# Kernel tuning notes

Hardware: AMD Instinct MI355X
Metric: run time of the kernel (lower is better)

Reference implementation:

```python
import jax, jax.numpy as jnp
import numpy as np

B, N, H = 32, 512, 256


def setup_inputs() -> dict:
    key = jax.random.key(0)
    ks = jax.random.split(key, 10)
    s = 1.0 / np.sqrt(H)
    return {
        "encoder_outputs": jax.random.normal(ks[0], (B, N, H), jnp.float32),
        "W_ih": jax.random.normal(ks[1], (4 * H, H), jnp.float32) * s,  # LSTMCell input weights (i,f,g,o)
        "W_hh": jax.random.normal(ks[2], (4 * H, H), jnp.float32) * s,
        "b_ih": jnp.zeros((4 * H,), jnp.float32),
        "b_hh": jnp.zeros((4 * H,), jnp.float32),
        "W_a": jax.random.normal(ks[3], (H, H), jnp.float32) * s,  # attn_W_a (no bias)
        "U_a": jax.random.normal(ks[4], (H, H), jnp.float32) * s,  # attn_U_a (no bias)
        "v_a": jax.random.normal(ks[5], (H,), jnp.float32) * s,    # attn_v (H -> 1, no bias)
        "start_token": jax.random.uniform(ks[6], (H,), jnp.float32, -0.1, 0.1),
        "end_token": jax.random.uniform(ks[7], (H,), jnp.float32, -0.1, 0.1),
    }


def lstm_cell(x, h, c, W_ih, b_ih, W_hh, b_hh):
    gates = x @ W_ih.T + b_ih + h @ W_hh.T + b_hh  # [B, 4H], torch gate order i,f,g,o
    i, f, g, o = jnp.split(gates, 4, axis=-1)
    c2 = jax.nn.sigmoid(f) * c + jax.nn.sigmoid(i) * jnp.tanh(g)
    h2 = jax.nn.sigmoid(o) * jnp.tanh(c2)
    return h2, c2


def reference(encoder_outputs, W_ih, W_hh, b_ih, b_hh, W_a, U_a, v_a, start_token, end_token):
    batch, n_nodes, hidden = encoder_outputs.shape
    T = n_nodes + 1  # inference path: max_decoding_steps = num_input_nodes + 1
    # extended encoder outputs = [enc, end_token]; precompute W_a projection once
    ext = jnp.concatenate(
        [encoder_outputs, jnp.broadcast_to(end_token, (batch, 1, hidden))], axis=1
    )  # [B, T, H]
    enc_proj = jnp.einsum("bnh,kh->bnk", ext, W_a)  # [B, T, H]
    bidx = jnp.arange(batch)

    dec_in0 = jnp.broadcast_to(start_token, (batch, hidden))
    hx0 = jnp.zeros((batch, hidden), encoder_outputs.dtype)
    cx0 = jnp.zeros_like(hx0)
    mask0 = jnp.zeros((batch, T), encoder_outputs.dtype)

    def step(carry, _):
        dec_in, hx, cx, mask = carry
        hx, cx = lstm_cell(dec_in, hx, cx, W_ih, b_ih, W_hh, b_hh)
        q = hx @ U_a.T  # [B, H]
        scores = jnp.tanh(enc_proj + q[:, None, :]) @ v_a  # [B, T]
        scores = jnp.where(mask == 1, -jnp.inf, scores)
        scores = scores - jnp.max(scores, axis=1, keepdims=True)
        log_probs = jax.nn.log_softmax(scores, axis=1)  # [B, T]
        next_idx = jnp.argmax(log_probs, axis=1)  # greedy (no teacher forcing)
        sel = next_idx < n_nodes  # end token (idx == n_nodes) never gets masked
        mask = mask.at[bidx, next_idx].max(sel.astype(mask.dtype))
        gathered = encoder_outputs[bidx, jnp.minimum(next_idx, n_nodes - 1)]  # [B, H]
        dec_in = jnp.where(sel[:, None], gathered, end_token)
        return (dec_in, hx, cx, mask), (log_probs, next_idx)

    _, (outputs, selected) = jax.lax.scan(step, (dec_in0, hx0, cx0, mask0), None, length=T)
    return jnp.swapaxes(outputs, 0, 1), jnp.swapaxes(selected, 0, 1)  # [B,T,T], [B,T]
```

## Files before the change

kernel.cpp:

```cpp
#include <hip/hip_runtime.h>
#include <math.h>


#define NEG_BIG  (-1.0e30f)
#define SENTINEL (-3.0e38f)
#define L2E 1.4426950408889634f
#define C2T 2.8853900817779268f
#define LN2 0.6931471805599453f

#define OFF_CW   ((size_t)0)
#define OFF_ENCP ((size_t)327680)
#define OFF_BSUM ((size_t)4530176)
#define OFF_XW   ((size_t)4531200)
#define WS_END   ((size_t)21373952)
#define NEED_XW_BYTES (WS_END * 4)
#define SEL_OFF  ((size_t)(32u * 513u * 513u))

__device__ __forceinline__ float frcp(float x)  { float r; asm("v_rcp_f32 %0, %1" : "=v"(r) : "v"(x)); return r; }
__device__ __forceinline__ float fexp2(float x) { float r; asm("v_exp_f32 %0, %1" : "=v"(r) : "v"(x)); return r; }
__device__ __forceinline__ float flog2(float x) { float r; asm("v_log_f32 %0, %1" : "=v"(r) : "v"(x)); return r; }
__device__ __forceinline__ float fsig(float x)  { return frcp(1.f + fexp2(-L2E * x)); }
__device__ __forceinline__ float ftanh2(float x){ return fmaf(-2.f, frcp(fexp2(C2T * x) + 1.f), 1.f); }

__device__ __forceinline__ void bar_lgkm() {
  asm volatile("s_waitcnt lgkmcnt(0)\n\ts_barrier" ::: "memory");
}
__device__ __forceinline__ void bar_full() {
  asm volatile("s_waitcnt vmcnt(0) lgkmcnt(0)\n\ts_barrier" ::: "memory");
}

extern "C" __global__ void __launch_bounds__(256)
pd_proj(const float* __restrict__ enc,  const float* __restrict__ Wih,
        const float* __restrict__ Whh,  const float* __restrict__ bih,
        const float* __restrict__ bhh,  const float* __restrict__ Wa,
        const float* __restrict__ Ua,   const float* __restrict__ stok,
        const float* __restrict__ etok, float* __restrict__ ws, int ntA)
{
  __shared__ __align__(16) float smem[4352];
  const int tid = threadIdx.x;
  int bb = blockIdx.x;

  if (bb < ntA + 1028) {
    const bool isA = bb < ntA;
    const int tile = isA ? bb : bb - ntA;
    const int nTN  = isA ? 16 : 4;
    const int mt = tile / nTN, nt = tile % nTN;
    const int m0 = mt * 64, c0 = nt * 64;
    const float* Bmat = isA ? Wih : Wa;

    const int m_l = tid >> 2, kq = tid & 3;
    const int mrow = m0 + m_l;
    const int bA = mrow / 514, nA = mrow - bA * 514;
    const float* arow = (nA < 512) ? (enc + ((size_t)bA * 512 + nA) * 256)
                                   : (nA == 512 ? etok : stok);
    const float* brow = Bmat + (size_t)(c0 + m_l) * 256;
    float* As = smem; float* Bs = smem + 2176;
    const int ty = tid >> 4, tx = tid & 15;
    float acc[4][4] = {};

    for (int kc = 0; kc < 256; kc += 32) {
      __syncthreads();
      float4 a0 = ((const float4*)(arow + kc))[kq];
      float4 a1 = ((const float4*)(arow + kc))[kq + 4];
      float4 b0 = ((const float4*)(brow + kc))[kq];
      float4 b1 = ((const float4*)(brow + kc))[kq + 4];
      const int k0a = kq * 4;
      As[(k0a+0)*68 + m_l] = a0.x; As[(k0a+1)*68 + m_l] = a0.y;
      As[(k0a+2)*68 + m_l] = a0.z; As[(k0a+3)*68 + m_l] = a0.w;
      As[(16+k0a+0)*68 + m_l] = a1.x; As[(16+k0a+1)*68 + m_l] = a1.y;
      As[(16+k0a+2)*68 + m_l] = a1.z; As[(16+k0a+3)*68 + m_l] = a1.w;
      Bs[(k0a+0)*68 + m_l] = b0.x; Bs[(k0a+1)*68 + m_l] = b0.y;
      Bs[(k0a+2)*68 + m_l] = b0.z; Bs[(k0a+3)*68 + m_l] = b0.w;
      Bs[(16+k0a+0)*68 + m_l] = b1.x; Bs[(16+k0a+1)*68 + m_l] = b1.y;
      Bs[(16+k0a+2)*68 + m_l] = b1.z; Bs[(16+k0a+3)*68 + m_l] = b1.w;
      __syncthreads();
      #pragma unroll
      for (int k = 0; k < 32; ++k) {
        float4 a4 = *(const float4*)(As + k*68 + ty*4);
        float4 b4 = *(const float4*)(Bs + k*68 + tx*4);
        acc[0][0] = fmaf(a4.x, b4.x, acc[0][0]); acc[0][1] = fmaf(a4.x, b4.y, acc[0][1]);
        acc[0][2] = fmaf(a4.x, b4.z, acc[0][2]); acc[0][3] = fmaf(a4.x, b4.w, acc[0][3]);
        acc[1][0] = fmaf(a4.y, b4.x, acc[1][0]); acc[1][1] = fmaf(a4.y, b4.y, acc[1][1]);
        acc[1][2] = fmaf(a4.y, b4.z, acc[1][2]); acc[1][3] = fmaf(a4.y, b4.w, acc[1][3]);
        acc[2][0] = fmaf(a4.z, b4.x, acc[2][0]); acc[2][1] = fmaf(a4.z, b4.y, acc[2][1]);
        acc[2][2] = fmaf(a4.z, b4.z, acc[2][2]); acc[2][3] = fmaf(a4.z, b4.w, acc[2][3]);
        acc[3][0] = fmaf(a4.w, b4.x, acc[3][0]); acc[3][1] = fmaf(a4.w, b4.y, acc[3][1]);
        acc[3][2] = fmaf(a4.w, b4.z, acc[3][2]); acc[3][3] = fmaf(a4.w, b4.w, acc[3][3]);
      }
    }
    if (isA) {
      float b0 = bih[c0+tx*4+0] + bhh[c0+tx*4+0];
      float b1 = bih[c0+tx*4+1] + bhh[c0+tx*4+1];
      float b2 = bih[c0+tx*4+2] + bhh[c0+tx*4+2];
      float b3 = bih[c0+tx*4+3] + bhh[c0+tx*4+3];
      #pragma unroll
      for (int i = 0; i < 4; ++i) {
        int m = m0 + ty*4 + i; int bq = m / 514, n = m - bq * 514;
        float* d = ws + OFF_XW + ((size_t)bq*514 + n)*1024 + c0 + tx*4;
        d[0] = acc[i][0] + b0; d[1] = acc[i][1] + b1;
        d[2] = acc[i][2] + b2; d[3] = acc[i][3] + b3;
      }
    } else {
      #pragma unroll
      for (int i = 0; i < 4; ++i) {
        int m = m0 + ty*4 + i; int bq = m / 514, n = m - bq * 514;
        if (n < 513) {
          #pragma unroll
          for (int jj = 0; jj < 4; ++jj) {
            int j = c0 + tx*4 + jj;
            ws[OFF_ENCP + ((size_t)bq*256 + j)*513 + n] = fexp2(C2T * acc[i][jj]);
          }
        }
      }
    }
    return;
  }
  bb -= ntA + 1028;
  if (bb < 64) {
    const int kt = bb >> 4, rt = bb & 15;
    const int k0 = kt*64, r0 = rt*64;
    const int cl = tid & 63, rq = tid >> 6;
    for (int i = 0; i < 16; ++i) {
      int r = rq*16 + i;
      smem[r*65 + cl] = Whh[(size_t)(r0 + r)*256 + k0 + cl];
    }
    __syncthreads();
    for (int i = 0; i < 16; ++i) {
      int kk = k0 + rq*16 + i;
      ws[OFF_CW + (size_t)(kk >> 2)*5120 + (size_t)(r0 + cl)*4 + (kk & 3)]
          = smem[cl*65 + (rq*16 + i)];
    }
    return;
  }
  bb -= 64;
  if (bb < 16) {
    const int kt = bb >> 2, jt = bb & 3;
    const int k0 = kt*64, j0 = jt*64;
    const int cl = tid & 63, rq = tid >> 6;
    for (int i = 0; i < 16; ++i) {
      int j = rq*16 + i;
      smem[j*65 + cl] = Ua[(size_t)(j0 + j)*256 + k0 + cl];
    }
    __syncthreads();
    for (int i = 0; i < 16; ++i) {
      int kk = k0 + rq*16 + i;
      ws[OFF_CW + (size_t)(kk >> 2)*5120 + (size_t)(1024 + j0 + cl)*4 + (kk & 3)]
          = C2T * smem[cl*65 + (rq*16 + i)];
    }
    return;
  }
  for (int g = 0; g < 4; ++g)
    ws[OFF_BSUM + g*256 + tid] = bih[g*256 + tid] + bhh[g*256 + tid];
}

template<int USE_XW>
__global__ void __launch_bounds__(1024)
pd_decode(const float* __restrict__ enc, const float* __restrict__ Wih,
          const float* __restrict__ va,  const float* __restrict__ stok,
          const float* __restrict__ etok,
          float* __restrict__ out, float* __restrict__ ws)
{
  __shared__ __align__(16) float h_s[256];
  __shared__ __align__(16) float gpart[1024];
  __shared__ __align__(16) float qbuf[256];
  __shared__ __align__(16) float vbuf[256];
  __shared__ float maskb[513];
  __shared__ float spart[1040];
  __shared__ float redv[16];
  __shared__ int   redi[16];
  __shared__ int   sel_sh;
  __shared__ int   sel_flag;
  __shared__ int   cnt;

  const int tid  = threadIdx.x;
  const int b    = blockIdx.x;
  const int lane = tid & 63, w = tid >> 6;
  const float* cw = ws + OFF_CW;

  if (tid < 256) { h_s[tid] = 0.f; vbuf[tid] = va[tid]; }
  if (tid < 513) maskb[tid] = 0.f;
  gpart[tid] = 0.f;
  if (tid == 0) { sel_sh = 513; sel_flag = 0; cnt = 0; }
  float c_reg = 0.f;
  float bs0 = 0.f, bs1 = 0.f, bs2 = 0.f, bs3 = 0.f;
  if (!USE_XW && tid < 256) {
    bs0 = ws[OFF_BSUM + tid];       bs1 = ws[OFF_BSUM + 256 + tid];
    bs2 = ws[OFF_BSUM + 512 + tid]; bs3 = ws[OFF_BSUM + 768 + tid];
  }
  __syncthreads();

  const int nS = tid & 511, sS = tid >> 9;
  float sv = 0.f;
  #pragma unroll
  for (int j = 0; j < 32; ++j) {
    float4 v4 = *(const float4*)(vbuf + sS*128 + j*4);
    sv += v4.x + v4.y + v4.z + v4.w;
  }

  for (int t = 0; t < 513; ++t) {
    if (tid < 256) {
      int spins = 0;
      while (*(volatile int*)&sel_flag < t && ++spins < (1 << 22)) {}
      __threadfence_block();
      const int sel = *(volatile int*)&sel_sh;
      float xg0, xg1, xg2, xg3;
      if (USE_XW) {
        const float* xr = ws + OFF_XW + ((size_t)b*514 + sel)*1024 + tid;
        xg0 = xr[0]; xg1 = xr[256]; xg2 = xr[512]; xg3 = xr[768];
      } else {
        const float* xrow = (sel < 512) ? enc + ((size_t)b*512 + sel)*256
                                        : (sel == 512 ? etok : stok);
        const float4* x4 = (const float4*)xrow;
        xg0 = bs0; xg1 = bs1; xg2 = bs2; xg3 = bs3;
        #pragma unroll 2
        for (int k4 = 0; k4 < 64; ++k4) {
          float4 xv = x4[k4];
          float4 w0 = *(const float4*)(Wih + ((size_t)(tid      ))*256 + k4*4);
          float4 w1 = *(const float4*)(Wih + ((size_t)(256 + tid))*256 + k4*4);
          float4 w2 = *(const float4*)(Wih + ((size_t)(512 + tid))*256 + k4*4);
          float4 w3 = *(const float4*)(Wih + ((size_t)(768 + tid))*256 + k4*4);
          xg0 = fmaf(w0.x,xv.x,fmaf(w0.y,xv.y,fmaf(w0.z,xv.z,fmaf(w0.w,xv.w,xg0))));
          xg1 = fmaf(w1.x,xv.x,fmaf(w1.y,xv.y,fmaf(w1.z,xv.z,fmaf(w1.w,xv.w,xg1))));
          xg2 = fmaf(w2.x,xv.x,fmaf(w2.y,xv.y,fmaf(w2.z,xv.z,fmaf(w2.w,xv.w,xg2))));
          xg3 = fmaf(w3.x,xv.x,fmaf(w3.y,xv.y,fmaf(w3.z,xv.z,fmaf(w3.w,xv.w,xg3))));
        }
      }
      const float g0 = xg0 + gpart[tid];
      const float g1 = xg1 + gpart[256 + tid];
      const float g2 = xg2 + gpart[512 + tid];
      const float g3 = xg3 + gpart[768 + tid];
      const float cn = fsig(g1)*c_reg + fsig(g0)*ftanh2(g2);
      c_reg = cn;
      h_s[tid] = fsig(g3)*ftanh2(cn);
    }
    bar_lgkm();

    {
      float acc = 0.f;
      #pragma unroll 4
      for (int k4 = 0; k4 < 64; ++k4) {
        float4 h4 = *(const float4*)(h_s + k4*4);
        float4 wv = *(const float4*)(cw + (size_t)k4*5120 + (size_t)tid*4);
        acc = fmaf(wv.x,h4.x,fmaf(wv.y,h4.y,fmaf(wv.z,h4.z,fmaf(wv.w,h4.w,acc))));
      }
      gpart[tid] = acc;
      if (tid < 256) {
        float acc2 = 0.f;
        #pragma unroll 4
        for (int k4 = 0; k4 < 64; ++k4) {
          float4 h4 = *(const float4*)(h_s + k4*4);
          float4 wv = *(const float4*)(cw + (size_t)k4*5120 + (size_t)(1024 + tid)*4);
          acc2 = fmaf(wv.x,h4.x,fmaf(wv.y,h4.y,fmaf(wv.z,h4.z,fmaf(wv.w,h4.w,acc2))));
        }
        qbuf[tid] = fexp2(acc2);
      }
    }
    bar_lgkm();

    {
      const float* ET = ws + OFF_ENCP + ((size_t)b*256 + sS*128)*513 + nS;
      float sacc = 0.f;
      #pragma unroll 4
      for (int j4 = 0; j4 < 32; ++j4) {
        float4 F4 = *(const float4*)(qbuf + sS*128 + j4*4);
        float4 V4 = *(const float4*)(vbuf + sS*128 + j4*4);
        float e0 = ET[(size_t)(j4*4+0)*513];
        float e1 = ET[(size_t)(j4*4+1)*513];
        float e2 = ET[(size_t)(j4*4+2)*513];
        float e3 = ET[(size_t)(j4*4+3)*513];
        sacc = fmaf(V4.x, frcp(fmaf(e0, F4.x, 1.f)), sacc);
        sacc = fmaf(V4.y, frcp(fmaf(e1, F4.y, 1.f)), sacc);
        sacc = fmaf(V4.z, frcp(fmaf(e2, F4.z, 1.f)), sacc);
        sacc = fmaf(V4.w, frcp(fmaf(e3, F4.w, 1.f)), sacc);
      }
      spart[sS*520 + nS] = fmaf(-2.f, sacc, sv);
    }
    if (w == 0 || w == 8) {
      const int ss = w >> 3;
      const int j0 = ss*128 + lane*2;
      const float* er = ws + OFF_ENCP + ((size_t)b*256 + j0)*513 + 512;
      float a = vbuf[j0]   * frcp(fmaf(er[0],   qbuf[j0],   1.f))
              + vbuf[j0+1] * frcp(fmaf(er[513], qbuf[j0+1], 1.f));
      #pragma unroll
      for (int off = 1; off < 64; off <<= 1) a += __shfl_xor(a, off);
      if (lane == 0) spart[ss*520 + 512] = fmaf(-2.f, a, sv);
    }
    bar_lgkm();

    float val; int idx = tid;
    if (tid < 513) {
      float sc = spart[tid] + spart[520 + tid];
      if (maskb[tid] != 0.f) sc = NEG_BIG;
      out[((size_t)b*513 + t)*513 + tid] = sc;
      val = sc;
    } else val = SENTINEL;
    #pragma unroll
    for (int off = 1; off < 64; off <<= 1) {
      const float ov = __shfl_xor(val, off);
      const int   oi = __shfl_xor(idx, off);
      if (ov > val || (ov == val && oi < idx)) { val = ov; idx = oi; }
    }
    if (lane == 0) {
      redv[w] = val; redi[w] = idx;
      __threadfence_block();
      const int old = atomicAdd(&cnt, 1);
      if (old == 16*(t+1) - 1) {
        float bv = redv[0]; int bi = redi[0];
        #pragma unroll
        for (int w2 = 1; w2 < 16; ++w2) {
          const float ov = redv[w2]; const int oi = redi[w2];
          if (ov > bv || (ov == bv && oi < bi)) { bv = ov; bi = oi; }
        }
        sel_sh = bi;
        if (bi < 512) maskb[bi] = 1.f;
        out[SEL_OFF + (size_t)b*513 + t] = (float)bi;
        __threadfence_block();
        *(volatile int*)&sel_flag = t + 1;
      }
    }
  }

  bar_full();

  for (int r = w; r < 513; r += 16) {
    float* base = out + ((size_t)b*513 + r)*513;
    float v[9];
    #pragma unroll
    for (int j = 0; j < 8; ++j) v[j] = base[lane + j*64];
    v[8] = (lane == 0) ? base[512] : SENTINEL;
    float m = v[0];
    #pragma unroll
    for (int j = 1; j < 9; ++j) m = fmaxf(m, v[j]);
    #pragma unroll
    for (int off = 1; off < 64; off <<= 1) m = fmaxf(m, __shfl_xor(m, off));
    float z = 0.f;
    #pragma unroll
    for (int j = 0; j < 9; ++j) z += fexp2((v[j] - m) * L2E);
    #pragma unroll
    for (int off = 1; off < 64; off <<= 1) z += __shfl_xor(z, off);
    const float lse = m + flog2(z) * LN2;
    #pragma unroll
    for (int j = 0; j < 8; ++j) base[lane + j*64] = v[j] - lse;
    if (lane == 0) base[512] = v[8] - lse;
  }
}

extern "C" void kernel_launch(void* const* d_in, const int* in_sizes, int n_in,
                              void* d_out, int out_size, void* d_ws, size_t ws_size,
                              hipStream_t stream) {
  const float* enc  = (const float*)d_in[0];
  const float* Wih  = (const float*)d_in[1];
  const float* Whh  = (const float*)d_in[2];
  const float* bih  = (const float*)d_in[3];
  const float* bhh  = (const float*)d_in[4];
  const float* Wa   = (const float*)d_in[5];
  const float* Ua   = (const float*)d_in[6];
  const float* va   = (const float*)d_in[7];
  const float* stok = (const float*)d_in[8];
  const float* etok = (const float*)d_in[9];
  (void)in_sizes; (void)n_in; (void)out_size;

  const bool use_xw = ws_size >= NEED_XW_BYTES;
  const int ntA = use_xw ? 257 * 16 : 0;
  const int grid_pro = ntA + 1028 + 64 + 16 + 1;

  pd_proj<<<dim3(grid_pro), dim3(256), 0, stream>>>(
      enc, Wih, Whh, bih, bhh, Wa, Ua, stok, etok, (float*)d_ws, ntA);
  if (use_xw)
    pd_decode<1><<<dim3(32), dim3(1024), 0, stream>>>(
        enc, Wih, va, stok, etok, (float*)d_out, (float*)d_ws);
  else
    pd_decode<0><<<dim3(32), dim3(1024), 0, stream>>>(
        enc, Wih, va, stok, etok, (float*)d_out, (float*)d_ws);
}
```

Before: 8.785 ms.

## Use fp16 weights and encoder projections, cache recurrent weights, skip masked nodes

```diff
diff --git a/kernel.cpp b/kernel.cpp
--- a/kernel.cpp
+++ b/kernel.cpp
@@ -8,19 +8,34 @@
 #define C2T 2.8853900817779268f
 #define LN2 0.6931471805599453f
 
-#define OFF_CW   ((size_t)0)
-#define OFF_ENCP ((size_t)327680)
-#define OFF_BSUM ((size_t)4530176)
-#define OFF_XW   ((size_t)4531200)
-#define WS_END   ((size_t)21373952)
+typedef _Float16 h2t __attribute__((ext_vector_type(2)));
+
+#define OFF_WHP  ((size_t)0)
+#define OFF_EH   ((size_t)163840)
+#define OFF_BSUM ((size_t)2265088)
+#define OFF_XW   ((size_t)2266112)
+#define WS_END   (OFF_XW + (size_t)32*514*1024)
 #define NEED_XW_BYTES (WS_END * 4)
-#define SEL_OFF  ((size_t)(32u * 513u * 513u))
+#define SEL_OFF  ((size_t)(32u*513u*513u))
 
 __device__ __forceinline__ float frcp(float x)  { float r; asm("v_rcp_f32 %0, %1" : "=v"(r) : "v"(x)); return r; }
 __device__ __forceinline__ float fexp2(float x) { float r; asm("v_exp_f32 %0, %1" : "=v"(r) : "v"(x)); return r; }
 __device__ __forceinline__ float flog2(float x) { float r; asm("v_log_f32 %0, %1" : "=v"(r) : "v"(x)); return r; }
 __device__ __forceinline__ float fsig(float x)  { return frcp(1.f + fexp2(-L2E * x)); }
 __device__ __forceinline__ float ftanh2(float x){ return fmaf(-2.f, frcp(fexp2(C2T * x) + 1.f), 1.f); }
+
+__device__ __forceinline__ float fdot2u(uint a, uint b, float c) {
+  return __builtin_amdgcn_fdot2(__builtin_bit_cast(h2t, a),
+                                __builtin_bit_cast(h2t, b), c, false);
+}
+__device__ __forceinline__ uint pkh(float a, float b) {
+  h2t v; v[0] = (_Float16)a; v[1] = (_Float16)b;
+  return __builtin_bit_cast(uint, v);
+}
+__device__ __forceinline__ float2 cvt2(uint u) {
+  h2t v = __builtin_bit_cast(h2t, u);
+  float2 r; r.x = (float)v[0]; r.y = (float)v[1]; return r;
+}
 
 __device__ __forceinline__ void bar_lgkm() {
   asm volatile("s_waitcnt lgkmcnt(0)\n\ts_barrier" ::: "memory");
@@ -101,52 +116,40 @@
         d[2] = acc[i][2] + b2; d[3] = acc[i][3] + b3;
       }
     } else {
+      _Float16* eh = (_Float16*)(ws + OFF_EH);
       #pragma unroll
       for (int i = 0; i < 4; ++i) {
         int m = m0 + ty*4 + i; int bq = m / 514, n = m - bq * 514;
         if (n < 513) {
-          #pragma unroll
-          for (int jj = 0; jj < 4; ++jj) {
-            int j = c0 + tx*4 + jj;
-            ws[OFF_ENCP + ((size_t)bq*256 + j)*513 + n] = fexp2(C2T * acc[i][jj]);
-          }
+          _Float16* d = eh + ((size_t)bq*513 + n)*256 + c0 + tx*4;
+          d[0] = (_Float16)fexp2(C2T * acc[i][0]);
+          d[1] = (_Float16)fexp2(C2T * acc[i][1]);
+          d[2] = (_Float16)fexp2(C2T * acc[i][2]);
+          d[3] = (_Float16)fexp2(C2T * acc[i][3]);
         }
       }
     }
     return;
   }
   bb -= ntA + 1028;
-  if (bb < 64) {
-    const int kt = bb >> 4, rt = bb & 15;
-    const int k0 = kt*64, r0 = rt*64;
-    const int cl = tid & 63, rq = tid >> 6;
-    for (int i = 0; i < 16; ++i) {
-      int r = rq*16 + i;
-      smem[r*65 + cl] = Whh[(size_t)(r0 + r)*256 + k0 + cl];
-    }
-    __syncthreads();
-    for (int i = 0; i < 16; ++i) {
-      int kk = k0 + rq*16 + i;
-      ws[OFF_CW + (size_t)(kk >> 2)*5120 + (size_t)(r0 + cl)*4 + (kk & 3)]
-          = smem[cl*65 + (rq*16 + i)];
-    }
-    return;
-  }
-  bb -= 64;
-  if (bb < 16) {
-    const int kt = bb >> 2, jt = bb & 3;
-    const int k0 = kt*64, j0 = jt*64;
-    const int cl = tid & 63, rq = tid >> 6;
-    for (int i = 0; i < 16; ++i) {
-      int j = rq*16 + i;
-      smem[j*65 + cl] = Ua[(size_t)(j0 + j)*256 + k0 + cl];
-    }
-    __syncthreads();
-    for (int i = 0; i < 16; ++i) {
-      int kk = k0 + rq*16 + i;
-      ws[OFF_CW + (size_t)(kk >> 2)*5120 + (size_t)(1024 + j0 + cl)*4 + (kk & 3)]
-          = C2T * smem[cl*65 + (rq*16 + i)];
-    }
+  if (bb < 160) {
+    const int item = bb * 256 + tid;
+    const int pp = item / 640, rr = item - pp * 640;
+    float4 r0, r1;
+    if (rr < 512) {
+      r0 = *(const float4*)(Whh + (size_t)(2*rr  )*256 + 4*pp);
+      r1 = *(const float4*)(Whh + (size_t)(2*rr+1)*256 + 4*pp);
+    } else {
+      const int j2 = rr - 512;
+      float4 a = *(const float4*)(Ua + (size_t)(2*j2  )*256 + 4*pp);
+      float4 c = *(const float4*)(Ua + (size_t)(2*j2+1)*256 + 4*pp);
+      r0.x = C2T*a.x; r0.y = C2T*a.y; r0.z = C2T*a.z; r0.w = C2T*a.w;
+      r1.x = C2T*c.x; r1.y = C2T*c.y; r1.z = C2T*c.z; r1.w = C2T*c.w;
+    }
+    uint4 w;
+    w.x = pkh(r0.x, r0.y); w.y = pkh(r1.x, r1.y);
+    w.z = pkh(r0.z, r0.w); w.w = pkh(r1.z, r1.w);
+    ((uint4*)(ws + OFF_WHP))[(size_t)pp*640 + rr] = w;
     return;
   }
   for (int g = 0; g < 4; ++g)
@@ -154,33 +157,41 @@
 }
 
 template<int USE_XW>
-__global__ void __launch_bounds__(1024)
+__global__ void __launch_bounds__(1024, 4)
 pd_decode(const float* __restrict__ enc, const float* __restrict__ Wih,
           const float* __restrict__ va,  const float* __restrict__ stok,
           const float* __restrict__ etok,
           float* __restrict__ out, float* __restrict__ ws)
 {
-  __shared__ __align__(16) float h_s[256];
-  __shared__ __align__(16) float gpart[1024];
+  __shared__ __align__(16) uint4 whl4[12*640];
+  __shared__ __align__(16) uint  hh2[128];
+  __shared__ __align__(16) float gpf[1024];
   __shared__ __align__(16) float qbuf[256];
   __shared__ __align__(16) float vbuf[256];
-  __shared__ float maskb[513];
-  __shared__ float spart[1040];
+  __shared__ float cur_row[513];
+  __shared__ short actn[520];
+  __shared__ short posn[520];
   __shared__ float redv[16];
   __shared__ int   redi[16];
-  __shared__ int   sel_sh;
-  __shared__ int   sel_flag;
-  __shared__ int   cnt;
+  __shared__ int   sel_sh, sel_flag, cnt16, cnt_act;
 
   const int tid  = threadIdx.x;
   const int b    = blockIdx.x;
   const int lane = tid & 63, w = tid >> 6;
-  const float* cw = ws + OFF_CW;
-
-  if (tid < 256) { h_s[tid] = 0.f; vbuf[tid] = va[tid]; }
-  if (tid < 513) maskb[tid] = 0.f;
-  gpart[tid] = 0.f;
-  if (tid == 0) { sel_sh = 513; sel_flag = 0; cnt = 0; }
+  const uint4*  whp4g = (const uint4*)(ws + OFF_WHP);
+  const ushort* ehg   = (const ushort*)(ws + OFF_EH);
+
+  if (tid < 256) vbuf[tid] = va[tid];
+  if (tid < 513) { actn[tid] = (short)tid; posn[tid] = (short)tid; }
+  gpf[tid] = 0.f;
+  if (tid == 0) { sel_sh = 513; sel_flag = 0; cnt16 = 0; cnt_act = 513; }
+  for (int i = tid; i < 12*640; i += 1024)
+    whl4[i] = whp4g[(size_t)(14 + i/640)*640 + (i - (i/640)*640)];
+  uint4 wreg[14];
+  if (tid < 640) {
+    #pragma unroll
+    for (int pp = 0; pp < 14; ++pp) wreg[pp] = whp4g[(size_t)pp*640 + tid];
+  }
   float c_reg = 0.f;
   float bs0 = 0.f, bs1 = 0.f, bs2 = 0.f, bs3 = 0.f;
   if (!USE_XW && tid < 256) {
@@ -188,12 +199,10 @@
     bs2 = ws[OFF_BSUM + 512 + tid]; bs3 = ws[OFF_BSUM + 768 + tid];
   }
   __syncthreads();
-
-  const int nS = tid & 511, sS = tid >> 9;
   float sv = 0.f;
   #pragma unroll
-  for (int j = 0; j < 32; ++j) {
-    float4 v4 = *(const float4*)(vbuf + sS*128 + j*4);
+  for (int j = 0; j < 64; ++j) {
+    float4 v4 = *(const float4*)(vbuf + j*4);
     sv += v4.x + v4.y + v4.z + v4.w;
   }
 
@@ -225,72 +234,74 @@
           xg3 = fmaf(w3.x,xv.x,fmaf(w3.y,xv.y,fmaf(w3.z,xv.z,fmaf(w3.w,xv.w,xg3))));
         }
       }
-      const float g0 = xg0 + gpart[tid];
-      const float g1 = xg1 + gpart[256 + tid];
-      const float g2 = xg2 + gpart[512 + tid];
-      const float g3 = xg3 + gpart[768 + tid];
+      const float g0 = xg0 + gpf[tid];
+      const float g1 = xg1 + gpf[256 + tid];
+      const float g2 = xg2 + gpf[512 + tid];
+      const float g3 = xg3 + gpf[768 + tid];
       const float cn = fsig(g1)*c_reg + fsig(g0)*ftanh2(g2);
       c_reg = cn;
-      h_s[tid] = fsig(g3)*ftanh2(cn);
+      const float hv = fsig(g3)*ftanh2(cn);
+      const float hn = __shfl_down(hv, 1);
+      if (!(tid & 1))
+        hh2[tid >> 1] = __builtin_bit_cast(uint, __builtin_amdgcn_cvt_pkrtz(hv, hn));
     }
     bar_lgkm();
 
+    if (tid < 640) {
+      float a0 = 0.f, a1 = 0.f;
+      #pragma unroll
+      for (int pp = 0; pp < 64; ++pp) {
+        uint4 wv;
+        if (pp < 14)      wv = wreg[pp];
+        else if (pp < 26) wv = whl4[(pp-14)*640 + tid];
+        else              wv = whp4g[(size_t)pp*640 + tid];
+        const uint2 hh = *(const uint2*)(hh2 + 2*pp);
+        a0 = fdot2u(wv.x, hh.x, a0); a1 = fdot2u(wv.y, hh.x, a1);
+        a0 = fdot2u(wv.z, hh.y, a0); a1 = fdot2u(wv.w, hh.y, a1);
+      }
+      if (tid < 512) {
+        float2 g2v; g2v.x = a0; g2v.y = a1;
+        *(float2*)(gpf + 2*tid) = g2v;
+      } else {
+        const int j0 = 2*(tid - 512);
+        qbuf[j0]     = fexp2(a0);
+        qbuf[j0 + 1] = fexp2(a1);
+      }
+    }
+    bar_lgkm();
+
     {
-      float acc = 0.f;
-      #pragma unroll 4
-      for (int k4 = 0; k4 < 64; ++k4) {
-        float4 h4 = *(const float4*)(h_s + k4*4);
-        float4 wv = *(const float4*)(cw + (size_t)k4*5120 + (size_t)tid*4);
-        acc = fmaf(wv.x,h4.x,fmaf(wv.y,h4.y,fmaf(wv.z,h4.z,fmaf(wv.w,h4.w,acc))));
-      }
-      gpart[tid] = acc;
-      if (tid < 256) {
-        float acc2 = 0.f;
+      const int nact = cnt_act;
+      if (tid < nact) {
+        const int n = actn[tid];
+        const uint4* er = (const uint4*)(ehg + ((size_t)b*513 + n)*256);
+        float sacc = 0.f;
         #pragma unroll 4
-        for (int k4 = 0; k4 < 64; ++k4) {
-          float4 h4 = *(const float4*)(h_s + k4*4);
-          float4 wv = *(const float4*)(cw + (size_t)k4*5120 + (size_t)(1024 + tid)*4);
-          acc2 = fmaf(wv.x,h4.x,fmaf(wv.y,h4.y,fmaf(wv.z,h4.z,fmaf(wv.w,h4.w,acc2))));
-        }
-        qbuf[tid] = fexp2(acc2);
-      }
-    }
-    bar_lgkm();
-
-    {
-      const float* ET = ws + OFF_ENCP + ((size_t)b*256 + sS*128)*513 + nS;
-      float sacc = 0.f;
-      #pragma unroll 4
-      for (int j4 = 0; j4 < 32; ++j4) {
-        float4 F4 = *(const float4*)(qbuf + sS*128 + j4*4);
-        float4 V4 = *(const float4*)(vbuf + sS*128 + j4*4);
-        float e0 = ET[(size_t)(j4*4+0)*513];
-        float e1 = ET[(size_t)(j4*4+1)*513];
-        float e2 = ET[(size_t)(j4*4+2)*513];
-        float e3 = ET[(size_t)(j4*4+3)*513];
-        sacc = fmaf(V4.x, frcp(fmaf(e0, F4.x, 1.f)), sacc);
-        sacc = fmaf(V4.y, frcp(fmaf(e1, F4.y, 1.f)), sacc);
-        sacc = fmaf(V4.z, frcp(fmaf(e2, F4.z, 1.f)), sacc);
-        sacc = fmaf(V4.w, frcp(fmaf(e3, F4.w, 1.f)), sacc);
-      }
-      spart[sS*520 + nS] = fmaf(-2.f, sacc, sv);
-    }
-    if (w == 0 || w == 8) {
-      const int ss = w >> 3;
-      const int j0 = ss*128 + lane*2;
-      const float* er = ws + OFF_ENCP + ((size_t)b*256 + j0)*513 + 512;
-      float a = vbuf[j0]   * frcp(fmaf(er[0],   qbuf[j0],   1.f))
-              + vbuf[j0+1] * frcp(fmaf(er[513], qbuf[j0+1], 1.f));
-      #pragma unroll
-      for (int off = 1; off < 64; off <<= 1) a += __shfl_xor(a, off);
-      if (lane == 0) spart[ss*520 + 512] = fmaf(-2.f, a, sv);
+        for (int i = 0; i < 32; ++i) {
+          const uint4 e4 = er[i];
+          const float4 fA = *(const float4*)(qbuf + 8*i);
+          const float4 fB = *(const float4*)(qbuf + 8*i + 4);
+          const float4 vA = *(const float4*)(vbuf + 8*i);
+          const float4 vB = *(const float4*)(vbuf + 8*i + 4);
+          const float2 e0 = cvt2(e4.x), e1 = cvt2(e4.y);
+          const float2 e2 = cvt2(e4.z), e3 = cvt2(e4.w);
+          sacc = fmaf(vA.x, frcp(fmaf(e0.x, fA.x, 1.f)), sacc);
+          sacc = fmaf(vA.y, frcp(fmaf(e0.y, fA.y, 1.f)), sacc);
+          sacc = fmaf(vA.z, frcp(fmaf(e1.x, fA.z, 1.f)), sacc);
+          sacc = fmaf(vA.w, frcp(fmaf(e1.y, fA.w, 1.f)), sacc);
+          sacc = fmaf(vB.x, frcp(fmaf(e2.x, fB.x, 1.f)), sacc);
+          sacc = fmaf(vB.y, frcp(fmaf(e2.y, fB.y, 1.f)), sacc);
+          sacc = fmaf(vB.z, frcp(fmaf(e3.x, fB.z, 1.f)), sacc);
+          sacc = fmaf(vB.w, frcp(fmaf(e3.y, fB.w, 1.f)), sacc);
+        }
+        cur_row[n] = fmaf(-2.f, sacc, sv);
+      }
     }
     bar_lgkm();
 
     float val; int idx = tid;
     if (tid < 513) {
-      float sc = spart[tid] + spart[520 + tid];
-      if (maskb[tid] != 0.f) sc = NEG_BIG;
+      const float sc = cur_row[tid];
       out[((size_t)b*513 + t)*513 + tid] = sc;
       val = sc;
     } else val = SENTINEL;
@@ -303,7 +314,7 @@
     if (lane == 0) {
       redv[w] = val; redi[w] = idx;
       __threadfence_block();
-      const int old = atomicAdd(&cnt, 1);
+      const int old = atomicAdd(&cnt16, 1);
       if (old == 16*(t+1) - 1) {
         float bv = redv[0]; int bi = redi[0];
         #pragma unroll
@@ -312,7 +323,14 @@
           if (ov > bv || (ov == bv && oi < bi)) { bv = ov; bi = oi; }
         }
         sel_sh = bi;
-        if (bi < 512) maskb[bi] = 1.f;
+        if (bi < 512) {
+          cur_row[bi] = NEG_BIG;
+          const int p = posn[bi];
+          const int last = actn[cnt_act - 1];
+          actn[p] = (short)last;
+          posn[last] = (short)p;
+          cnt_act = cnt_act - 1;
+        }
         out[SEL_OFF + (size_t)b*513 + t] = (float)bi;
         __threadfence_block();
         *(volatile int*)&sel_flag = t + 1;
@@ -362,7 +380,7 @@
 
   const bool use_xw = ws_size >= NEED_XW_BYTES;
   const int ntA = use_xw ? 257 * 16 : 0;
-  const int grid_pro = ntA + 1028 + 64 + 16 + 1;
+  const int grid_pro = ntA + 1028 + 160 + 1;
 
   pd_proj<<<dim3(grid_pro), dim3(256), 0, stream>>>(
       enc, Wih, Whh, bih, bhh, Wa, Ua, stok, etok, (float*)d_ws, ntA);
```

Result: no change. 8.955 ms (+1.9%).
